# Kernel optimization log

Measured on AMD Instinct MI355X. Metric: run time of the kernel, lower is better.

The kernel has to match this reference:

```python
import jax, jax.numpy as jnp
from jax import lax
import numpy as np

N_CLASS = 5
B, T = 2048, 2048


def setup_inputs() -> dict:
    key = jax.random.key(0)
    k1, k2 = jax.random.split(key)
    x = jax.random.normal(k1, (B, T, N_CLASS), dtype=jnp.float32)
    mask = jnp.ones((B, T), dtype=jnp.int32)
    transform = jax.random.normal(k2, (N_CLASS + 2, N_CLASS + 2), dtype=jnp.float32)
    return {"x": x, "mask": mask, "transform": transform}


def reference(x, mask, transform):
    # Batched Viterbi decode. x:[B,T,C], mask:[B,T], transform:[C+2,C+2]
    Bb, Tt, C = x.shape
    START, END = C, C + 1
    trans = transform[:C, :C]                      # [C,C] prev -> curr
    mb = mask.astype(bool)

    dp0 = x[:, 0, :] + transform[START, :C][None]  # [B,C]

    def step(dp, inp):
        xt, mt = inp                               # xt:[B,C], mt:[B]
        sc = dp[:, :, None] + trans[None]          # [B,C_prev,C_curr]
        bp = jnp.argmax(sc, axis=1)                # [B,C]
        new_dp = jnp.max(sc, axis=1) + xt          # [B,C]
        dp_out = jnp.where(mt[:, None], new_dp, dp)
        # identity backpointer on padded steps so backtrace is a no-op there
        bp_out = jnp.where(mt[:, None], bp, jnp.arange(C)[None, :])
        return dp_out, bp_out

    xs = (jnp.moveaxis(x[:, 1:, :], 1, 0),         # [T-1,B,C]
          jnp.moveaxis(mb[:, 1:], 1, 0))           # [T-1,B]
    dp, bps = lax.scan(step, dp0, xs)              # bps: [T-1,B,C]

    final = dp + transform[:C, END][None]          # [B,C]
    max_score = jnp.max(final, axis=1)             # [B]
    last = jnp.argmax(final, axis=1)               # [B]

    def back(idx, bp):
        prev = jnp.take_along_axis(bp, idx[:, None], axis=1)[:, 0]
        return prev, idx

    first, rest = lax.scan(back, last, bps, reverse=True)  # rest: [T-1,B]
    path = jnp.concatenate([first[None], rest], axis=0)    # [T,B]
    return max_score, path.T                                # [B], [B,T]
```

## Files before the change

### kernel.cpp

```cpp
#include <hip/hip_runtime.h>
#include <cstdint>

#define B_ 2048
#define T_ 2048
#define TD 7
#define IDENT 0x4688u

__device__ __forceinline__ uint32_t mcompose(uint32_t f, uint32_t g) {
    uint32_t r = 0;
#pragma unroll
    for (int j = 0; j < 5; ++j) {
        uint32_t gj = (g >> (3 * j)) & 7u;
        r |= ((f >> (3 * gj)) & 7u) << (3 * j);
    }
    return r;
}

__device__ __forceinline__ uint32_t cvtpk(float lo, float hi) {
    uint32_t r;
    asm("v_cvt_pk_bf16_f32 %0, %1, %2" : "=v"(r) : "v"(lo), "v"(hi));
    return r;
}
__device__ __forceinline__ float blo(uint32_t w) { return __uint_as_float(w << 16); }
__device__ __forceinline__ float bhi(uint32_t w) { return __uint_as_float(w & 0xFFFF0000u); }

__device__ __forceinline__ void hstep5(float x0, float x1, float x2, float x3, float x4,
                                       bool mm, float (&dp)[5], const float (&tr)[5][5]) {
    const float xx[5] = {x0, x1, x2, x3, x4};
    float nd[5];
#pragma unroll
    for (int j = 0; j < 5; ++j) {
        float v = fmaxf(fmaxf(fmaxf(fmaxf(dp[0] + tr[0][j], dp[1] + tr[1][j]),
                                    dp[2] + tr[2][j]), dp[3] + tr[3][j]),
                        dp[4] + tr[4][j]);
        nd[j] = v + xx[j];
    }
#pragma unroll
    for (int j = 0; j < 5; ++j) dp[j] = mm ? nd[j] : dp[j];
}

__device__ __forceinline__ uint32_t vstep5(float x0, float x1, float x2, float x3, float x4,
                                           bool mm, float (&dp)[5], const float (&tr)[5][5]) {
    const float xx[5] = {x0, x1, x2, x3, x4};
    float nd[5]; uint32_t pk = 0;
#pragma unroll
    for (int j = 0; j < 5; ++j) {
        float s[5];
#pragma unroll
        for (int i = 0; i < 5; ++i) {
            float f = dp[i] + tr[i][j];
            s[i] = __uint_as_float((__float_as_uint(f) & ~7u) | (uint32_t)(7 - i));
        }
        float m = fmaxf(fmaxf(fmaxf(fmaxf(s[0], s[1]), s[2]), s[3]), s[4]);
        int a = 7 - (int)(__float_as_uint(m) & 7u);
        float v = m + xx[j];
        a = mm ? a : j;
        nd[j] = mm ? v : dp[j];
        pk |= ((uint32_t)a) << (3 * j);
    }
#pragma unroll
    for (int j = 0; j < 5; ++j) dp[j] = nd[j];
    return pk;
}

__global__ __launch_bounds__(64) void k_all(
    const float* __restrict__ x, const int* __restrict__ mask,
    const float* __restrict__ tf, float* __restrict__ out, uint32_t* __restrict__ ws)
{
    __shared__ __align__(16) uint16_t xs[10240];
    uint32_t* xs32 = (uint32_t*)xs;
    const int b = blockIdx.x, c = threadIdx.x;

    const float4* gx = (const float4*)(x + (size_t)b * (T_ * 5));

#pragma unroll
    for (int qo = 0; qo < 5; ++qo) {
        float4 v[8];
#pragma unroll
        for (int u = 0; u < 8; ++u) v[u] = gx[c + 64 * (8 * qo + u)];
#pragma unroll
        for (int u = 0; u < 8; ++u) {
            uint32_t e0 = 4u * (uint32_t)c + 256u * (uint32_t)(8 * qo + u);
            uint32_t co = e0 / 160u;
            uint32_t k  = (e0 - 160u * co) >> 1;
            uint32_t sw = (co >> 1) & 15u;
            xs32[80u * co + (k ^ sw)]        = cvtpk(v[u].x, v[u].y);
            xs32[80u * co + ((k + 1u) ^ sw)] = cvtpk(v[u].z, v[u].w);
        }
    }

    uint32_t mb = 0;
    {
        const int4* gmc = (const int4*)(mask + (size_t)b * T_ + 32 * c);
        int4 m[8];
#pragma unroll
        for (int u = 0; u < 8; ++u) m[u] = gmc[u];
#pragma unroll
        for (int u = 0; u < 8; ++u) {
            mb |= (m[u].x ? 1u : 0u) << (4 * u);
            mb |= (m[u].y ? 1u : 0u) << (4 * u + 1);
            mb |= (m[u].z ? 1u : 0u) << (4 * u + 2);
            mb |= (m[u].w ? 1u : 0u) << (4 * u + 3);
        }
    }

    float tr[5][5], ts[5], te[5];
#pragma unroll
    for (int i = 0; i < 5; ++i)
#pragma unroll
        for (int j = 0; j < 5; ++j) tr[i][j] = tf[i * TD + j];
#pragma unroll
    for (int j = 0; j < 5; ++j) ts[j] = tf[5 * TD + j];
#pragma unroll
    for (int j = 0; j < 5; ++j) te[j] = tf[j * TD + 6];

    uint32_t mh = __shfl_up(mb, 1);
    mh = (c > 0) ? (mh >> 16) : 0u;
    if (c == 0) mb &= ~1u;

    __syncthreads();

    const int hc = (c > 0) ? c - 1 : 0;
    const uint32_t swl = (uint32_t)((c >> 1) & 15);
    const uint32_t swh = (uint32_t)((hc >> 1) & 15);
    const uint32_t* xl = xs32 + 80 * c;
    const uint32_t* xh = xs32 + 80 * hc;

    float dp[5];
    {
        uint32_t w0 = xh[40u ^ swh], w1 = xh[41u ^ swh], w2 = xh[42u ^ swh];
        dp[0] = blo(w0); dp[1] = bhi(w0); dp[2] = blo(w1); dp[3] = bhi(w1); dp[4] = blo(w2);
    }
    for (int hi = 0; hi < 7; ++hi) {
        uint32_t d0 = (uint32_t)(42 + 5 * hi);
        uint32_t w0 = xh[(d0 + 0u) ^ swh], w1 = xh[(d0 + 1u) ^ swh], w2 = xh[(d0 + 2u) ^ swh];
        uint32_t w3 = xh[(d0 + 3u) ^ swh], w4 = xh[(d0 + 4u) ^ swh], w5 = xh[(d0 + 5u) ^ swh];
        bool m1 = ((mh >> (2 * hi + 1)) & 1u) != 0;
        bool m2 = ((mh >> (2 * hi + 2)) & 1u) != 0;
        hstep5(bhi(w0), blo(w1), bhi(w1), blo(w2), bhi(w2), m1, dp, tr);
        hstep5(blo(w3), bhi(w3), blo(w4), bhi(w4), blo(w5), m2, dp, tr);
    }
    {
        uint32_t w0 = xh[77u ^ swh], w1 = xh[78u ^ swh], w2 = xh[79u ^ swh];
        bool m1 = ((mh >> 15) & 1u) != 0;
        hstep5(bhi(w0), blo(w1), bhi(w1), blo(w2), bhi(w2), m1, dp, tr);
    }
    if (c == 0) {
        uint32_t w0 = xs32[0], w1 = xs32[1], w2 = xs32[2];
        dp[0] = blo(w0) + ts[0]; dp[1] = bhi(w0) + ts[1];
        dp[2] = blo(w1) + ts[2]; dp[3] = bhi(w1) + ts[3];
        dp[4] = blo(w2) + ts[4];
    }
    float dpE[5];
#pragma unroll
    for (int j = 0; j < 5; ++j) dpE[j] = (c == 0) ? 0.0f : dp[j];

    uint32_t rho = IDENT;
    uint32_t* wrow = ws + ((size_t)b << 10) + c;
    for (int it = 0; it < 16; ++it) {
        uint32_t d0 = (uint32_t)(5 * it);
        uint32_t w0 = xl[(d0 + 0u) ^ swl], w1 = xl[(d0 + 1u) ^ swl], w2 = xl[(d0 + 2u) ^ swl];
        uint32_t w3 = xl[(d0 + 3u) ^ swl], w4 = xl[(d0 + 4u) ^ swl];
        bool mA = ((mb >> (2 * it)) & 1u) != 0;
        bool mB = ((mb >> (2 * it + 1)) & 1u) != 0;
        uint32_t pkA = vstep5(blo(w0), bhi(w0), blo(w1), bhi(w1), blo(w2), mA, dp, tr);
        rho = mcompose(rho, pkA);
        uint32_t pkB = vstep5(bhi(w2), blo(w3), bhi(w3), blo(w4), bhi(w4), mB, dp, tr);
        rho = mcompose(rho, pkB);
        wrow[it * 64] = pkA | (pkB << 16);
    }

    float svec[5];
#pragma unroll
    for (int j = 0; j < 5; ++j) {
        int r = (rho >> (3 * j)) & 7;
        float e = dpE[0];
        e = (r == 1) ? dpE[1] : e;
        e = (r == 2) ? dpE[2] : e;
        e = (r == 3) ? dpE[3] : e;
        e = (r == 4) ? dpE[4] : e;
        svec[j] = dp[j] - e;
    }

    uint32_t I = rho;
#pragma unroll
    for (int d = 1; d < 64; d <<= 1) {
        uint32_t oth = __shfl_down(I, d);
        uint32_t cm  = mcompose(I, oth);
        I = (c + d < 64) ? cm : I;
    }
    float best = dp[0] + te[0]; int lastv = 0;
#pragma unroll
    for (int j = 1; j < 5; ++j) {
        float s = dp[j] + te[j];
        if (s > best) { best = s; lastv = j; }
    }
    const int last = __shfl(lastv, 63);
    uint32_t M = __shfl_down(I, 1);
    M = (c < 63) ? M : IDENT;
    const int ec = (int)((M >> (3 * last)) & 7u);

    {
        float v = svec[0];
        v = (ec == 1) ? svec[1] : v;
        v = (ec == 2) ? svec[2] : v;
        v = (ec == 3) ? svec[3] : v;
        v = (ec == 4) ? svec[4] : v;
        if (c == 63) v += te[last];
#pragma unroll
        for (int off = 1; off < 64; off <<= 1) v += __shfl_xor(v, off);
        if (c == 0) out[b] = v;
    }

    const uint32_t* rrow = ws + ((size_t)b << 10) + c;
    float* path = out + B_ + (size_t)b * T_ + 32 * c;
    int e = ec;
    for (int dd = 3; dd >= 0; --dd) {
        uint32_t q0 = rrow[(4 * dd + 0) * 64], q1 = rrow[(4 * dd + 1) * 64];
        uint32_t q2 = rrow[(4 * dd + 2) * 64], q3 = rrow[(4 * dd + 3) * 64];
        float pv[8];
        {
            uint32_t pB = q3 >> 16, pA = q3 & 0xFFFFu;
            pv[7] = (float)e; e = (int)((pB >> (3 * e)) & 7u);
            pv[6] = (float)e; e = (int)((pA >> (3 * e)) & 7u);
        }
        {
            uint32_t pB = q2 >> 16, pA = q2 & 0xFFFFu;
            pv[5] = (float)e; e = (int)((pB >> (3 * e)) & 7u);
            pv[4] = (float)e; e = (int)((pA >> (3 * e)) & 7u);
        }
        {
            uint32_t pB = q1 >> 16, pA = q1 & 0xFFFFu;
            pv[3] = (float)e; e = (int)((pB >> (3 * e)) & 7u);
            pv[2] = (float)e; e = (int)((pA >> (3 * e)) & 7u);
        }
        {
            uint32_t pB = q0 >> 16, pA = q0 & 0xFFFFu;
            pv[1] = (float)e; e = (int)((pB >> (3 * e)) & 7u);
            pv[0] = (float)e; e = (int)((pA >> (3 * e)) & 7u);
        }
        float4 s0; s0.x = pv[0]; s0.y = pv[1]; s0.z = pv[2]; s0.w = pv[3];
        float4 s1; s1.x = pv[4]; s1.y = pv[5]; s1.z = pv[6]; s1.w = pv[7];
        ((float4*)path)[2 * dd]     = s0;
        ((float4*)path)[2 * dd + 1] = s1;
    }
}

extern "C" void kernel_launch(void* const* d_in, const int* in_sizes, int n_in,
                              void* d_out, int out_size, void* d_ws, size_t ws_size,
                              hipStream_t stream) {
    const float* x         = (const float*)d_in[0];
    const int*   mask      = (const int*)d_in[1];
    const float* transform = (const float*)d_in[2];
    float*       out       = (float*)d_out;
    uint32_t*    ws        = (uint32_t*)d_ws;

    hipLaunchKernelGGL(k_all, dim3(B_), dim3(64), 0, stream,
                       x, mask, transform, out, ws);
}
```

Baseline: 40.53 us.

## Process two rows per block with register-prefetched second row and register backpointers

```diff
diff --git a/kernel.cpp b/kernel.cpp
--- a/kernel.cpp
+++ b/kernel.cpp
@@ -63,62 +63,38 @@
     return pk;
 }
 
-__global__ __launch_bounds__(64) void k_all(
-    const float* __restrict__ x, const int* __restrict__ mask,
-    const float* __restrict__ tf, float* __restrict__ out, uint32_t* __restrict__ ws)
+__device__ __forceinline__ void stage_write(uint32_t* __restrict__ xs32, int c, int q,
+                                            const float4& v) {
+    uint32_t e0 = 4u * (uint32_t)(c + 64 * q);
+    uint32_t co = e0 / 160u;
+    uint32_t k  = (e0 - 160u * co) >> 1;
+    uint32_t sw = (co >> 1) & 15u;
+    xs32[80u * co + (k ^ sw)]        = cvtpk(v.x, v.y);
+    xs32[80u * co + ((k + 1u) ^ sw)] = cvtpk(v.z, v.w);
+}
+
+__device__ __forceinline__ uint32_t mask_bits8(const int4 (&m)[8]) {
+    uint32_t mb = 0;
+#pragma unroll
+    for (int u = 0; u < 8; ++u) {
+        mb |= (m[u].x ? 1u : 0u) << (4 * u);
+        mb |= (m[u].y ? 1u : 0u) << (4 * u + 1);
+        mb |= (m[u].z ? 1u : 0u) << (4 * u + 2);
+        mb |= (m[u].w ? 1u : 0u) << (4 * u + 3);
+    }
+    return mb;
+}
+
+template<bool PR>
+__device__ __forceinline__ void compute_row(
+    const uint32_t* __restrict__ xs32, uint32_t* __restrict__ xsB,
+    const float4 (&pf)[40], uint32_t mb, int b, int c,
+    const float (&tr)[5][5], const float (&ts)[5], const float (&te)[5],
+    float* __restrict__ out)
 {
-    __shared__ __align__(16) uint16_t xs[10240];
-    uint32_t* xs32 = (uint32_t*)xs;
-    const int b = blockIdx.x, c = threadIdx.x;
-
-    const float4* gx = (const float4*)(x + (size_t)b * (T_ * 5));
-
-#pragma unroll
-    for (int qo = 0; qo < 5; ++qo) {
-        float4 v[8];
-#pragma unroll
-        for (int u = 0; u < 8; ++u) v[u] = gx[c + 64 * (8 * qo + u)];
-#pragma unroll
-        for (int u = 0; u < 8; ++u) {
-            uint32_t e0 = 4u * (uint32_t)c + 256u * (uint32_t)(8 * qo + u);
-            uint32_t co = e0 / 160u;
-            uint32_t k  = (e0 - 160u * co) >> 1;
-            uint32_t sw = (co >> 1) & 15u;
-            xs32[80u * co + (k ^ sw)]        = cvtpk(v[u].x, v[u].y);
-            xs32[80u * co + ((k + 1u) ^ sw)] = cvtpk(v[u].z, v[u].w);
-        }
-    }
-
-    uint32_t mb = 0;
-    {
-        const int4* gmc = (const int4*)(mask + (size_t)b * T_ + 32 * c);
-        int4 m[8];
-#pragma unroll
-        for (int u = 0; u < 8; ++u) m[u] = gmc[u];
-#pragma unroll
-        for (int u = 0; u < 8; ++u) {
-            mb |= (m[u].x ? 1u : 0u) << (4 * u);
-            mb |= (m[u].y ? 1u : 0u) << (4 * u + 1);
-            mb |= (m[u].z ? 1u : 0u) << (4 * u + 2);
-            mb |= (m[u].w ? 1u : 0u) << (4 * u + 3);
-        }
-    }
-
-    float tr[5][5], ts[5], te[5];
-#pragma unroll
-    for (int i = 0; i < 5; ++i)
-#pragma unroll
-        for (int j = 0; j < 5; ++j) tr[i][j] = tf[i * TD + j];
-#pragma unroll
-    for (int j = 0; j < 5; ++j) ts[j] = tf[5 * TD + j];
-#pragma unroll
-    for (int j = 0; j < 5; ++j) te[j] = tf[j * TD + 6];
-
     uint32_t mh = __shfl_up(mb, 1);
     mh = (c > 0) ? (mh >> 16) : 0u;
     if (c == 0) mb &= ~1u;
-
-    __syncthreads();
 
     const int hc = (c > 0) ? c - 1 : 0;
     const uint32_t swl = (uint32_t)((c >> 1) & 15);
@@ -155,8 +131,14 @@
 #pragma unroll
     for (int j = 0; j < 5; ++j) dpE[j] = (c == 0) ? 0.0f : dp[j];
 
+    if constexpr (PR) {
+#pragma unroll
+        for (int q = 0; q < 10; ++q) stage_write(xsB, c, q, pf[q]);
+    }
+
+    uint32_t acc[16];
     uint32_t rho = IDENT;
-    uint32_t* wrow = ws + ((size_t)b << 10) + c;
+#pragma unroll
     for (int it = 0; it < 16; ++it) {
         uint32_t d0 = (uint32_t)(5 * it);
         uint32_t w0 = xl[(d0 + 0u) ^ swl], w1 = xl[(d0 + 1u) ^ swl], w2 = xl[(d0 + 2u) ^ swl];
@@ -167,7 +149,21 @@
         rho = mcompose(rho, pkA);
         uint32_t pkB = vstep5(bhi(w2), blo(w3), bhi(w3), blo(w4), bhi(w4), mB, dp, tr);
         rho = mcompose(rho, pkB);
-        wrow[it * 64] = pkA | (pkB << 16);
+        acc[it] = pkA | (pkB << 16);
+        if constexpr (PR) {
+            if (it == 4) {
+#pragma unroll
+                for (int q = 10; q < 20; ++q) stage_write(xsB, c, q, pf[q]);
+            }
+            if (it == 9) {
+#pragma unroll
+                for (int q = 20; q < 30; ++q) stage_write(xsB, c, q, pf[q]);
+            }
+            if (it == 14) {
+#pragma unroll
+                for (int q = 30; q < 40; ++q) stage_write(xsB, c, q, pf[q]);
+            }
+        }
     }
 
     float svec[5];
@@ -212,38 +208,75 @@
         if (c == 0) out[b] = v;
     }
 
-    const uint32_t* rrow = ws + ((size_t)b << 10) + c;
+    float pv[32];
+    int e = ec;
+#pragma unroll
+    for (int l = 31; l >= 0; --l) {
+        pv[l] = (float)e;
+        uint32_t p = (acc[l >> 1] >> (16 * (l & 1))) & 0xFFFFu;
+        e = (p >> (3 * e)) & 7;
+    }
     float* path = out + B_ + (size_t)b * T_ + 32 * c;
-    int e = ec;
-    for (int dd = 3; dd >= 0; --dd) {
-        uint32_t q0 = rrow[(4 * dd + 0) * 64], q1 = rrow[(4 * dd + 1) * 64];
-        uint32_t q2 = rrow[(4 * dd + 2) * 64], q3 = rrow[(4 * dd + 3) * 64];
-        float pv[8];
-        {
-            uint32_t pB = q3 >> 16, pA = q3 & 0xFFFFu;
-            pv[7] = (float)e; e = (int)((pB >> (3 * e)) & 7u);
-            pv[6] = (float)e; e = (int)((pA >> (3 * e)) & 7u);
-        }
-        {
-            uint32_t pB = q2 >> 16, pA = q2 & 0xFFFFu;
-            pv[5] = (float)e; e = (int)((pB >> (3 * e)) & 7u);
-            pv[4] = (float)e; e = (int)((pA >> (3 * e)) & 7u);
-        }
-        {
-            uint32_t pB = q1 >> 16, pA = q1 & 0xFFFFu;
-            pv[3] = (float)e; e = (int)((pB >> (3 * e)) & 7u);
-            pv[2] = (float)e; e = (int)((pA >> (3 * e)) & 7u);
-        }
-        {
-            uint32_t pB = q0 >> 16, pA = q0 & 0xFFFFu;
-            pv[1] = (float)e; e = (int)((pB >> (3 * e)) & 7u);
-            pv[0] = (float)e; e = (int)((pA >> (3 * e)) & 7u);
-        }
-        float4 s0; s0.x = pv[0]; s0.y = pv[1]; s0.z = pv[2]; s0.w = pv[3];
-        float4 s1; s1.x = pv[4]; s1.y = pv[5]; s1.z = pv[6]; s1.w = pv[7];
-        ((float4*)path)[2 * dd]     = s0;
-        ((float4*)path)[2 * dd + 1] = s1;
-    }
+#pragma unroll
+    for (int q = 0; q < 8; ++q) {
+        float4 v; v.x = pv[4*q]; v.y = pv[4*q+1]; v.z = pv[4*q+2]; v.w = pv[4*q+3];
+        ((float4*)path)[q] = v;
+    }
+}
+
+__global__ __launch_bounds__(64, 1) void k_all(
+    const float* __restrict__ x, const int* __restrict__ mask,
+    const float* __restrict__ tf, float* __restrict__ out)
+{
+    __shared__ __align__(16) uint32_t xsA[5120];
+    __shared__ __align__(16) uint32_t xsB[5120];
+    const int c = threadIdx.x;
+    const int b0 = 2 * blockIdx.x, b1 = b0 + 1;
+
+    const float4* gx0 = (const float4*)(x + (size_t)b0 * (T_ * 5));
+    const float4* gx1 = (const float4*)(x + (size_t)b1 * (T_ * 5));
+    const int4*   gm0 = (const int4*)(mask + (size_t)b0 * T_ + 32 * c);
+    const int4*   gm1 = (const int4*)(mask + (size_t)b1 * T_ + 32 * c);
+
+#pragma unroll
+    for (int qo = 0; qo < 5; ++qo) {
+        float4 v[8];
+#pragma unroll
+        for (int u = 0; u < 8; ++u) v[u] = gx0[c + 64 * (8 * qo + u)];
+#pragma unroll
+        for (int u = 0; u < 8; ++u) stage_write(xsA, c, 8 * qo + u, v[u]);
+    }
+    int4 m0[8];
+#pragma unroll
+    for (int u = 0; u < 8; ++u) m0[u] = gm0[u];
+    const uint32_t mb0 = mask_bits8(m0);
+
+    float tr[5][5], ts[5], te[5];
+#pragma unroll
+    for (int i = 0; i < 5; ++i)
+#pragma unroll
+        for (int j = 0; j < 5; ++j) tr[i][j] = tf[i * TD + j];
+#pragma unroll
+    for (int j = 0; j < 5; ++j) ts[j] = tf[5 * TD + j];
+#pragma unroll
+    for (int j = 0; j < 5; ++j) te[j] = tf[j * TD + 6];
+
+    __syncthreads();
+
+    float4 pf[40];
+#pragma unroll
+    for (int q = 0; q < 40; ++q) pf[q] = gx1[c + 64 * q];
+    int4 m1[8];
+#pragma unroll
+    for (int u = 0; u < 8; ++u) m1[u] = gm1[u];
+    __builtin_amdgcn_sched_barrier(0);
+
+    compute_row<true>(xsA, xsB, pf, mb0, b0, c, tr, ts, te, out);
+
+    const uint32_t mb1 = mask_bits8(m1);
+    __syncthreads();
+
+    compute_row<false>(xsB, xsA, pf, mb1, b1, c, tr, ts, te, out);
 }
 
 extern "C" void kernel_launch(void* const* d_in, const int* in_sizes, int n_in,
@@ -253,8 +286,7 @@
     const int*   mask      = (const int*)d_in[1];
     const float* transform = (const float*)d_in[2];
     float*       out       = (float*)d_out;
-    uint32_t*    ws        = (uint32_t*)d_ws;
-
-    hipLaunchKernelGGL(k_all, dim3(B_), dim3(64), 0, stream,
-                       x, mask, transform, out, ws);
-}
+
+    hipLaunchKernelGGL(k_all, dim3(B_ / 2), dim3(64), 0, stream,
+                       x, mask, transform, out);
+}
```

After: 45.66 us. 12.7% more time.
